# Kernel tuning notes

Hardware: AMD Instinct MI355X
Metric: run time of the kernel (lower is better)

## Reference

```python
import jax, jax.numpy as jnp
import numpy as np

B, N, G = 16, 6000, 256
T = 200                     # TRAIN_ROIS_PER_IMAGE
RATIO = 0.33                # POSITIVE_ROI_RATIO
POS_NUM = int(T * RATIO)    # 66 positive slots
NEG_SLOTS = T - POS_NUM     # 134 negative slots
BBOX_STD = jnp.asarray([0.1, 0.1, 0.2, 0.2], jnp.float32)
EPS = 1e-8


def _rand_boxes(key, b, n):
    # valid [y1,x1,y2,x2] boxes in [0,1]
    k1, k2 = jax.random.split(key)
    tl = jax.random.uniform(k1, (b, n, 2)) * 0.7
    wh = jax.random.uniform(k2, (b, n, 2)) * 0.25 + 0.02
    return jnp.concatenate([tl, tl + wh], axis=-1).astype(jnp.float32)


def setup_inputs() -> dict:
    key = jax.random.key(0)
    k1, k2, k3, k4, k5 = jax.random.split(key, 5)
    rois = _rand_boxes(k1, B, N)
    rois = rois.at[:, N - 1000:].set(0.0)          # zero padding tail (remove_zero_padding)
    gt_boxes = _rand_boxes(k2, B, G)
    gt_ids = jax.random.randint(k3, (B, G), 1, 81, dtype=jnp.int32)
    gt_ids = gt_ids.at[:, G - 32:G - 16].set(-1)   # crowd boxes (ids < 0)
    gt_ids = gt_ids.at[:, G - 16:].set(0)          # padded gt
    gt_boxes = gt_boxes.at[:, G - 16:].set(0.0)
    pos_score = jax.random.uniform(k4, (B, N), dtype=jnp.float32)
    neg_score = jax.random.uniform(k5, (B, N), dtype=jnp.float32)
    return {"rois": rois, "gt_ids": gt_ids, "gt_boxes": gt_boxes,
            "pos_score": pos_score, "neg_score": neg_score}


def _pairwise_iou(a, b):
    # a:[N,4], b:[G,4] -> [N,G]
    y1 = jnp.maximum(a[:, None, 0], b[None, :, 0])
    x1 = jnp.maximum(a[:, None, 1], b[None, :, 1])
    y2 = jnp.minimum(a[:, None, 2], b[None, :, 2])
    x2 = jnp.minimum(a[:, None, 3], b[None, :, 3])
    inter = jnp.clip(y2 - y1, 0.0) * jnp.clip(x2 - x1, 0.0)
    area_a = (a[:, 2] - a[:, 0]) * (a[:, 3] - a[:, 1])
    area_b = (b[:, 2] - b[:, 0]) * (b[:, 3] - b[:, 1])
    union = area_a[:, None] + area_b[None, :] - inter
    return inter / jnp.maximum(union, EPS)


def _bbox_offset(boxes, gt):
    h = jnp.maximum(boxes[:, 2] - boxes[:, 0], EPS)
    w = jnp.maximum(boxes[:, 3] - boxes[:, 1], EPS)
    cy = boxes[:, 0] + 0.5 * h
    cx = boxes[:, 1] + 0.5 * w
    gh = jnp.maximum(gt[:, 2] - gt[:, 0], EPS)
    gw = jnp.maximum(gt[:, 3] - gt[:, 1], EPS)
    gcy = gt[:, 0] + 0.5 * gh
    gcx = gt[:, 1] + 0.5 * gw
    off = jnp.stack([(gcy - cy) / h, (gcx - cx) / w,
                     jnp.log(gh / h), jnp.log(gw / w)], axis=1)
    return off / BBOX_STD


def _per_image(rois, gt_ids, gt_boxes, pos_score, neg_score):
    roi_valid = jnp.any(rois != 0.0, axis=1)        # [N]
    gt_valid = jnp.any(gt_boxes != 0.0, axis=1)     # [G]
    crowd = gt_valid & (gt_ids < 0)
    non_crowd = gt_valid & (gt_ids > 0)

    iou = _pairwise_iou(rois, gt_boxes)             # [N,G]
    iou_nc = jnp.where(non_crowd[None, :], iou, -1.0)
    iou_nc_max = jnp.max(iou_nc, axis=1)
    iou_cr_max = jnp.max(jnp.where(crowd[None, :], iou, 0.0), axis=1)

    pos_mask = roi_valid & (iou_nc_max >= 0.5)
    neg_mask = roi_valid & (iou_nc_max < 0.5) & (iou_cr_max < 0.001)

    # random sampling == sort by iid uniform scores (masked out -> -inf)
    pos_idx = jnp.argsort(-jnp.where(pos_mask, pos_score, -jnp.inf))[:POS_NUM]
    pos_count = jnp.minimum(jnp.sum(pos_mask), POS_NUM).astype(jnp.int32)
    pos_slot_valid = jnp.arange(POS_NUM) < pos_count

    neg_target = (jnp.float32(1.0 / RATIO) * pos_count.astype(jnp.float32)).astype(jnp.int32) - pos_count
    neg_idx = jnp.argsort(-jnp.where(neg_mask, neg_score, -jnp.inf))[:NEG_SLOTS]
    neg_count = jnp.minimum(jnp.sum(neg_mask).astype(jnp.int32),
                            jnp.minimum(neg_target, NEG_SLOTS))
    neg_slot_valid = jnp.arange(NEG_SLOTS) < neg_count

    pos_rois_raw = rois[pos_idx]                                   # [P,4]
    pos_rois = jnp.where(pos_slot_valid[:, None], pos_rois_raw, 0.0)
    neg_rois = jnp.where(neg_slot_valid[:, None], rois[neg_idx], 0.0)

    assign = jnp.argmax(iou_nc[pos_idx], axis=1)                   # gt assignment
    roi_gt_boxes = gt_boxes[assign]
    roi_gt_ids = jnp.where(pos_slot_valid, gt_ids[assign], 0)

    off = _bbox_offset(pos_rois_raw, roi_gt_boxes)
    off = jnp.where(pos_slot_valid[:, None], off, 0.0)

    out_rois = jnp.concatenate([pos_rois, neg_rois], axis=0)       # [T,4]
    out_ids = jnp.pad(roi_gt_ids, (0, NEG_SLOTS))                  # [T]
    out_off = jnp.pad(off, ((0, NEG_SLOTS), (0, 0)))               # [T,4]
    return out_rois, out_ids, out_off


def reference(rois, gt_ids, gt_boxes, pos_score, neg_score):
    return jax.vmap(_per_image)(rois, gt_ids, gt_boxes, pos_score, neg_score)
```

## Files before the change

kernel.cpp:

```cpp
#include <hip/hip_runtime.h>

#define BIMG 16
#define NROI 6000
#define NGT  256
#define TPOS 66
#define TNEG 134
#define TTOT 200
#define EPSF 1e-8f
#define INVALID_SCORE 0xFFFFFFFFu

#define CPB 2
#define UNITSB 94
#define P1_BLOCKS (UNITSB * BIMG)
#define NWAIT (2 * BIMG)
#define NT 256
#define VSLOTS 6
#define CAND_CAP 384

#define MAGIC1 0x9E3779B9u
#define MAGIC2 0x85EBCA77u

typedef unsigned long long u64;
typedef unsigned int u32;
typedef unsigned short u16;

struct P1Shared {
    float4 ncbox[NGT];
    float4 crbox[NGT];
    u16    gmap[NGT];
    int    wnc[4], wcr[4];
};

struct SelShared {
    u32 hist[2048];
    u32 wtot[4];
    u32 wsuf[4];
    int pick;
    u32 higher;
    u32 pickpop;
    u32 count;
    u64 comp[CAND_CAP];
    int cnt;
    int sel[TNEG];
};

__device__ __forceinline__ void phase1_block(
    int unit,
    const float* __restrict__ rois, const int* __restrict__ gt_ids,
    const float* __restrict__ gt_boxes, const float* __restrict__ pos_score,
    const float* __restrict__ neg_score, u32* __restrict__ pos_s,
    u32* __restrict__ neg_s, u32* __restrict__ assign, u32* __restrict__ flags,
    P1Shared& S)
{
#pragma clang fp contract(off)
    const int b = unit / UNITSB;
    const int u = unit - b * UNITSB;

    const int r_local = threadIdx.x >> 3;
    const int sub = threadIdx.x & 7;

    const float4* rois4 = (const float4*)rois + (size_t)b * NROI;
    float4 rbk[CPB];
    float  psk[CPB], nsk[CPB];
    int    nk[CPB];
#pragma unroll
    for (int k = 0; k < CPB; ++k) {
        int n = (u * CPB + k) * 32 + r_local;
        nk[k] = n;
        int ne = min(n, NROI - 1);
        rbk[k] = rois4[ne];
        psk[k] = 0.f; nsk[k] = 0.f;
        if (sub == 0) {
            psk[k] = pos_score[b * NROI + ne];
            nsk[k] = neg_score[b * NROI + ne];
        }
    }

    {
        const int g = threadIdx.x;
        const int lane = g & 63, w = g >> 6;
        float4 gb = ((const float4*)gt_boxes)[b * NGT + g];
        bool valid = (gb.x != 0.f) || (gb.y != 0.f) || (gb.z != 0.f) || (gb.w != 0.f);
        int id = gt_ids[b * NGT + g];
        bool isnc = valid && (id > 0);
        bool iscr = valid && (id < 0);
        u64 mnc = __ballot(isnc);
        u64 mcr = __ballot(iscr);
        if (lane == 0) { S.wnc[w] = (int)__popcll(mnc); S.wcr[w] = (int)__popcll(mcr); }
        __syncthreads();
        int offnc = 0, offcr = 0;
        for (int j = 0; j < w; ++j) { offnc += S.wnc[j]; offcr += S.wcr[j]; }
        u64 below = (lane == 0) ? 0ull : (~0ull >> (64 - lane));
        if (isnc) {
            int slot = offnc + (int)__popcll(mnc & below);
            S.ncbox[slot] = gb;
            S.gmap[slot] = (u16)g;
        }
        if (iscr) {
            int slot = offcr + (int)__popcll(mcr & below);
            S.crbox[slot] = gb;
        }
    }
    __syncthreads();
    const int nccnt = S.wnc[0] + S.wnc[1] + S.wnc[2] + S.wnc[3];
    const int crcnt = S.wcr[0] + S.wcr[1] + S.wcr[2] + S.wcr[3];

#pragma unroll
    for (int k = 0; k < CPB; ++k) {
        const float4 rb = rbk[k];
        const int n = nk[k];
        const bool rvalid = (rb.x != 0.f) || (rb.y != 0.f) || (rb.z != 0.f) || (rb.w != 0.f);
        const float area_a = (rb.z - rb.x) * (rb.w - rb.y);

        float best = -1.0f;
        float bsl  = 0.0f;
        float crmax = 0.0f;

        if (__ballot(rvalid) != 0ull) {
            auto step = [&](int i) {
                float4 p0 = S.ncbox[i];
                float y1 = fmaxf(rb.x, p0.x);
                float x1 = fmaxf(rb.y, p0.y);
                float y2 = fminf(rb.z, p0.z);
                float x2 = fminf(rb.w, p0.w);
                float ih = fmaxf(y2 - y1, 0.0f);
                float iw = fmaxf(x2 - x1, 0.0f);
                float inter = ih * iw;
                float ab = (p0.z - p0.x) * (p0.w - p0.y);
                float uni = fmaxf(area_a + ab - inter, EPSF);
                float iou = inter / uni;
                if (iou > best) { best = iou; bsl = (float)i; }
            };
            int i = sub;
            for (; i + 8 < nccnt; i += 16) { step(i); step(i + 8); }
            if (i < nccnt) step(i);

            for (int j = sub; j < crcnt; j += 8) {
                float4 p0 = S.crbox[j];
                float y1 = fmaxf(rb.x, p0.x);
                float x1 = fmaxf(rb.y, p0.y);
                float y2 = fminf(rb.z, p0.z);
                float x2 = fminf(rb.w, p0.w);
                float ih = fmaxf(y2 - y1, 0.0f);
                float iw = fmaxf(x2 - x1, 0.0f);
                float inter = ih * iw;
                float ab = (p0.z - p0.x) * (p0.w - p0.y);
                float uni = fmaxf(area_a + ab - inter, EPSF);
                crmax = fmaxf(crmax, inter / uni);
            }

            for (int m = 1; m <= 4; m <<= 1) {
                float ov = __shfl_xor(best, m);
                float os = __shfl_xor(bsl, m);
                float oc = __shfl_xor(crmax, m);
                if ((ov > best) || ((ov == best) && (os < bsl))) { best = ov; bsl = os; }
                crmax = fmaxf(crmax, oc);
            }
        }

        if (sub == 0 && n < NROI) {
            u32 ps = INVALID_SCORE, ns = INVALID_SCORE;
            if (rvalid) {
                if (best >= 0.5f)
                    ps = __float_as_uint(psk[k]);
                if ((best < 0.5f) && (crmax < 0.001f))
                    ns = __float_as_uint(nsk[k]);
            }
            int gsel = (nccnt > 0) ? (int)S.gmap[(int)bsl] : 0;
            __hip_atomic_store(&pos_s[b * NROI + n], ps,
                               __ATOMIC_RELAXED, __HIP_MEMORY_SCOPE_AGENT);
            __hip_atomic_store(&neg_s[b * NROI + n], ns,
                               __ATOMIC_RELAXED, __HIP_MEMORY_SCOPE_AGENT);
            __hip_atomic_store(&assign[b * NROI + n], (u32)gsel,
                               __ATOMIC_RELAXED, __HIP_MEMORY_SCOPE_AGENT);
        }
    }

    __syncthreads();
    if (threadIdx.x == 0) {
        __hip_atomic_store(&flags[2 * unit],     MAGIC1,
                           __ATOMIC_RELAXED, __HIP_MEMORY_SCOPE_AGENT);
        __hip_atomic_store(&flags[2 * unit + 1], MAGIC2,
                           __ATOMIC_RELAXED, __HIP_MEMORY_SCOPE_AGENT);
    }
}

__device__ __forceinline__ int count_valid(const u32* __restrict__ src,
                                           int tid, int lane, SelShared* S)
{
    const uint4* src4 = (const uint4*)src;
    int myvalid = 0;
#pragma unroll
    for (int s = 0; s < VSLOTS; ++s) {
        int vi = s * NT + tid;
        uint4 v = src4[vi];
        int base = vi * 4;
        myvalid += (base + 0 < NROI && v.x != INVALID_SCORE);
        myvalid += (base + 1 < NROI && v.y != INVALID_SCORE);
        myvalid += (base + 2 < NROI && v.z != INVALID_SCORE);
        myvalid += (base + 3 < NROI && v.w != INVALID_SCORE);
    }
    for (int off = 1; off < 64; off <<= 1) myvalid += __shfl_xor(myvalid, off);
    if (tid == 0) S->count = 0;
    __syncthreads();
    if (lane == 0) atomicAdd(&S->count, (u32)myvalid);
    __syncthreads();
    int tot = (int)S->count;
    __syncthreads();
    return tot;
}

__device__ __forceinline__ int radix_select(const u32* __restrict__ src, int K,
                                            int tid, int lane, int w, SelShared* S)
{
    const uint4* src4 = (const uint4*)src;
    int myvalid = 0;
#pragma unroll
    for (int s = 0; s < VSLOTS; ++s) {
        int vi = s * NT + tid;
        uint4 v = src4[vi];
        int base = vi * 4;
        myvalid += (base + 0 < NROI && v.x != INVALID_SCORE);
        myvalid += (base + 1 < NROI && v.y != INVALID_SCORE);
        myvalid += (base + 2 < NROI && v.z != INVALID_SCORE);
        myvalid += (base + 3 < NROI && v.w != INVALID_SCORE);
    }
    for (int off = 1; off < 64; off <<= 1) myvalid += __shfl_xor(myvalid, off);
    if (tid == 0) S->count = 0;
    __syncthreads();
    if (lane == 0) atomicAdd(&S->count, (u32)myvalid);
    __syncthreads();
    const int total = (int)S->count;
    const int K0 = min(K, total);
    if (K0 <= 0) return total;

    int Krem = K0;
    u64 prefix = 0ull, mask = 0ull;
    int cand = total;

    for (int p = 3; p >= 0; --p) {
        if (cand <= CAND_CAP) break;
        const int shift = p * 11;
        for (int i = tid; i < 2048; i += NT) S->hist[i] = 0;
        __syncthreads();
#pragma unroll
        for (int s = 0; s < VSLOTS; ++s) {
            int vi = s * NT + tid;
            uint4 v = src4[vi];
            int base = vi * 4;
            u32 vv[4] = {v.x, v.y, v.z, v.w};
#pragma unroll
            for (int j = 0; j < 4; ++j) {
                int idx = base + j;
                if (idx < NROI && vv[j] != INVALID_SCORE) {
                    u64 kk = ((u64)vv[j] << 13) | (u64)(8191 - idx);
                    if ((kk & mask) == prefix)
                        atomicAdd(&S->hist[(u32)(kk >> shift) & 2047u], 1u);
                }
            }
        }
        __syncthreads();
        u32 local = 0;
#pragma unroll
        for (int j = 0; j < 8; ++j) local += S->hist[8 * tid + j];
        u32 suf = local;
        for (int off = 1; off < 64; off <<= 1) {
            u32 v = __shfl_down(suf, off);
            if (lane + off < 64) suf += v;
        }
        if (lane == 0) S->wtot[w] = suf;
        __syncthreads();
        if (tid < 4) {
            u32 t = 0;
            for (int j = tid + 1; j < 4; ++j) t += S->wtot[j];
            S->wsuf[tid] = t;
        }
        __syncthreads();
        u32 Sincl = suf + S->wsuf[w];
        for (int k2 = 0; k2 < 8; ++k2) {
            u32 h = S->hist[8 * tid + k2];
            u32 Snext = Sincl - h;
            if (Sincl >= (u32)Krem && Snext < (u32)Krem) {
                S->pick = 8 * tid + k2;
                S->higher = Snext;
                S->pickpop = h;
            }
            Sincl = Snext;
        }
        __syncthreads();
        prefix |= ((u64)(u32)S->pick) << shift;
        mask   |= (2047ull << shift);
        Krem   -= (int)S->higher;
        cand    = (K0 - Krem) + (int)S->pickpop;
        __syncthreads();
    }

    if (tid == 0) S->cnt = 0;
    __syncthreads();
#pragma unroll
    for (int s = 0; s < VSLOTS; ++s) {
        int vi = s * NT + tid;
        uint4 v = src4[vi];
        int base = vi * 4;
        u32 vv[4] = {v.x, v.y, v.z, v.w};
#pragma unroll
        for (int j = 0; j < 4; ++j) {
            int idx = base + j;
            if (idx < NROI && vv[j] != INVALID_SCORE) {
                u64 kk = ((u64)vv[j] << 13) | (u64)(8191 - idx);
                if ((kk & mask) >= prefix) {
                    int pos = atomicAdd(&S->cnt, 1);
                    S->comp[pos] = kk;
                }
            }
        }
    }
    __syncthreads();
    const int Cnt = S->cnt;
    for (int c0 = tid; c0 < Cnt; c0 += NT) {
        u64 kk = S->comp[c0];
        int rank = 0;
        for (int j = 0; j < Cnt; ++j) rank += (S->comp[j] > kk);
        if (rank < K0) S->sel[rank] = 8191 - (int)(kk & 8191ull);
    }
    __syncthreads();
    return total;
}

__device__ __forceinline__ void phase2_block(
    int wbid,
    const float* __restrict__ rois, const int* __restrict__ gt_ids,
    const float* __restrict__ gt_boxes, const u32* __restrict__ pos_s,
    const u32* __restrict__ neg_s, const u32* __restrict__ assign,
    const u32* __restrict__ flags, float* __restrict__ out, SelShared& S)
{
#pragma clang fp contract(off)
    __shared__ int s_ndone;
    const int b = wbid >> 1;
    const int side = wbid & 1;
    const int tid = threadIdx.x;
    const int lane = tid & 63;
    const int w = tid >> 6;

    const u32* fb = flags + 2 * (b * UNITSB);
    int mydone = (tid < UNITSB) ? 0 : 1;
    for (;;) {
        if (tid == 0) s_ndone = 0;
        __syncthreads();
        if (!mydone) {
            u32 a = __hip_atomic_load(&fb[2 * tid],
                                      __ATOMIC_RELAXED, __HIP_MEMORY_SCOPE_AGENT);
            u32 c = __hip_atomic_load(&fb[2 * tid + 1],
                                      __ATOMIC_RELAXED, __HIP_MEMORY_SCOPE_AGENT);
            mydone = (a == MAGIC1 && c == MAGIC2);
        }
        int d = mydone;
        for (int off = 1; off < 64; off <<= 1) d += __shfl_xor(d, off);
        if (lane == 0) atomicAdd(&s_ndone, d);
        __syncthreads();
        if (s_ndone == NT) break;
        __builtin_amdgcn_s_sleep(8);
    }
    if (tid == 0)
        (void)__hip_atomic_load(&fb[0], __ATOMIC_ACQUIRE, __HIP_MEMORY_SCOPE_AGENT);
    __syncthreads();

    float* out_rois = out;
    float* out_ids  = out + BIMG * TTOT * 4;
    float* out_off  = out + BIMG * TTOT * 4 + BIMG * TTOT;

    if (side == 0) {
        const int pos_total = radix_select(pos_s + (size_t)b * NROI, TPOS,
                                           tid, lane, w, &S);
        const int pos_count = min(pos_total, TPOS);

        if (tid < TPOS) {
            const int base = b * TTOT + tid;
            float4 ro  = make_float4(0.f, 0.f, 0.f, 0.f);
            float  idv = 0.f;
            float4 off = make_float4(0.f, 0.f, 0.f, 0.f);
            if (tid < pos_count) {
                int n = S.sel[tid];
                float4 rb = ((const float4*)rois)[b * NROI + n];
                ro = rb;
                int g = (int)assign[b * NROI + n];
                float4 gb = ((const float4*)gt_boxes)[b * NGT + g];
                idv = (float)gt_ids[b * NGT + g];

                float h  = fmaxf(rb.z - rb.x, EPSF);
                float wd = fmaxf(rb.w - rb.y, EPSF);
                float cy = rb.x + 0.5f * h;
                float cx = rb.y + 0.5f * wd;
                float gh = fmaxf(gb.z - gb.x, EPSF);
                float gw = fmaxf(gb.w - gb.y, EPSF);
                float gcy = gb.x + 0.5f * gh;
                float gcx = gb.y + 0.5f * gw;
                off.x = ((gcy - cy) / h)  / 0.1f;
                off.y = ((gcx - cx) / wd) / 0.1f;
                off.z = logf(gh / h)  / 0.2f;
                off.w = logf(gw / wd) / 0.2f;
            }
            ((float4*)out_rois)[base] = ro;
            out_ids[base] = idv;
            ((float4*)out_off)[base] = off;
        }
    } else {
        const int pos_total = count_valid(pos_s + (size_t)b * NROI, tid, lane, &S);
        const int pos_count = min(pos_total, TPOS);
        const float ratio_inv = (float)(1.0 / 0.33);
        const int neg_target = (int)(ratio_inv * (float)pos_count) - pos_count;

        const int neg_total = radix_select(neg_s + (size_t)b * NROI, TNEG,
                                           tid, lane, w, &S);
        const int neg_count = max(0, min(neg_total, min(neg_target, TNEG)));

        if (tid < TNEG) {
            const int base = b * TTOT + TPOS + tid;
            float4 ro = make_float4(0.f, 0.f, 0.f, 0.f);
            if (tid < neg_count) {
                int n = S.sel[tid];
                ro = ((const float4*)rois)[b * NROI + n];
            }
            ((float4*)out_rois)[base] = ro;
            out_ids[base] = 0.f;
            ((float4*)out_off)[base] = make_float4(0.f, 0.f, 0.f, 0.f);
        }
    }
}

__global__ __launch_bounds__(NT, 4)
void fused_kernel(const float* __restrict__ rois,
                  const int* __restrict__ gt_ids,
                  const float* __restrict__ gt_boxes,
                  const float* __restrict__ pos_score,
                  const float* __restrict__ neg_score,
                  u32* __restrict__ pos_s,
                  u32* __restrict__ neg_s,
                  u32* __restrict__ assign,
                  u32* __restrict__ flags,
                  float* __restrict__ out)
{
    constexpr size_t SB = sizeof(P1Shared) > sizeof(SelShared)
                        ? sizeof(P1Shared) : sizeof(SelShared);
    __shared__ __align__(16) char smem[SB];

    if (blockIdx.x >= NWAIT) {
        phase1_block((int)blockIdx.x - NWAIT, rois, gt_ids, gt_boxes, pos_score,
                     neg_score, pos_s, neg_s, assign, flags,
                     *reinterpret_cast<P1Shared*>(smem));
    } else {
        phase2_block((int)blockIdx.x, rois, gt_ids, gt_boxes,
                     pos_s, neg_s, assign, flags, out,
                     *reinterpret_cast<SelShared*>(smem));
    }
}

extern "C" void kernel_launch(void* const* d_in, const int* in_sizes, int n_in,
                              void* d_out, int out_size, void* d_ws, size_t ws_size,
                              hipStream_t stream) {
    const float* rois      = (const float*)d_in[0];
    const int*   gt_ids    = (const int*)d_in[1];
    const float* gt_boxes  = (const float*)d_in[2];
    const float* pos_score = (const float*)d_in[3];
    const float* neg_score = (const float*)d_in[4];
    float* out = (float*)d_out;

    char* ws = (char*)d_ws;
    u32* pos_s  = (u32*)(ws + 0);
    u32* neg_s  = (u32*)(ws + 384000);
    u32* assign = (u32*)(ws + 768000);
    u32* flags  = (u32*)(ws + 1152000);

    fused_kernel<<<NWAIT + P1_BLOCKS, NT, 0, stream>>>(
        rois, gt_ids, gt_boxes, pos_score, neg_score,
        pos_s, neg_s, assign, flags, out);
}
```

Before: 96.76 us.

## Map one ROI per thread in phase 1 and precompute GT areas

Phase 1 now gives each thread a whole ROI and loops over all GT boxes itself, replacing the old scheme of 8 threads per ROI followed by a shuffle reduction. The number of phase-1 blocks per image falls from 94 to 24. GT box areas are computed once and stored in shared memory instead of being recomputed for every pair. This removes the shuffle reductions and the redundant area math, but it cuts block count and parallelism, so each thread runs a loop about 8x longer and the grid may not fill the GPU.

```diff
diff --git a/kernel.cpp b/kernel.cpp
--- a/kernel.cpp
+++ b/kernel.cpp
@@ -9,8 +9,8 @@
 #define EPSF 1e-8f
 #define INVALID_SCORE 0xFFFFFFFFu
 
-#define CPB 2
-#define UNITSB 94
+#define RPB 256
+#define UNITSB 24
 #define P1_BLOCKS (UNITSB * BIMG)
 #define NWAIT (2 * BIMG)
 #define NT 256
@@ -26,7 +26,9 @@
 
 struct P1Shared {
     float4 ncbox[NGT];
+    float  ncarea[NGT];
     float4 crbox[NGT];
+    float  crarea[NGT];
     u16    gmap[NGT];
     int    wnc[4], wcr[4];
 };
@@ -55,33 +57,21 @@
 #pragma clang fp contract(off)
     const int b = unit / UNITSB;
     const int u = unit - b * UNITSB;
-
-    const int r_local = threadIdx.x >> 3;
-    const int sub = threadIdx.x & 7;
-
-    const float4* rois4 = (const float4*)rois + (size_t)b * NROI;
-    float4 rbk[CPB];
-    float  psk[CPB], nsk[CPB];
-    int    nk[CPB];
-#pragma unroll
-    for (int k = 0; k < CPB; ++k) {
-        int n = (u * CPB + k) * 32 + r_local;
-        nk[k] = n;
-        int ne = min(n, NROI - 1);
-        rbk[k] = rois4[ne];
-        psk[k] = 0.f; nsk[k] = 0.f;
-        if (sub == 0) {
-            psk[k] = pos_score[b * NROI + ne];
-            nsk[k] = neg_score[b * NROI + ne];
-        }
-    }
+    const int tid = threadIdx.x;
+
+    const int n = u * RPB + tid;
+    const int ne = min(n, NROI - 1);
+    const float4 rb = ((const float4*)rois)[b * NROI + ne];
+    const float ps_in = pos_score[b * NROI + ne];
+    const float ns_in = neg_score[b * NROI + ne];
 
     {
-        const int g = threadIdx.x;
+        const int g = tid;
         const int lane = g & 63, w = g >> 6;
         float4 gb = ((const float4*)gt_boxes)[b * NGT + g];
         bool valid = (gb.x != 0.f) || (gb.y != 0.f) || (gb.z != 0.f) || (gb.w != 0.f);
         int id = gt_ids[b * NGT + g];
+        float area = (gb.z - gb.x) * (gb.w - gb.y);
         bool isnc = valid && (id > 0);
         bool iscr = valid && (id < 0);
         u64 mnc = __ballot(isnc);
@@ -94,90 +84,76 @@
         if (isnc) {
             int slot = offnc + (int)__popcll(mnc & below);
             S.ncbox[slot] = gb;
+            S.ncarea[slot] = area;
             S.gmap[slot] = (u16)g;
         }
         if (iscr) {
             int slot = offcr + (int)__popcll(mcr & below);
             S.crbox[slot] = gb;
+            S.crarea[slot] = area;
         }
     }
     __syncthreads();
     const int nccnt = S.wnc[0] + S.wnc[1] + S.wnc[2] + S.wnc[3];
     const int crcnt = S.wcr[0] + S.wcr[1] + S.wcr[2] + S.wcr[3];
 
-#pragma unroll
-    for (int k = 0; k < CPB; ++k) {
-        const float4 rb = rbk[k];
-        const int n = nk[k];
-        const bool rvalid = (rb.x != 0.f) || (rb.y != 0.f) || (rb.z != 0.f) || (rb.w != 0.f);
+    const bool rvalid = (rb.x != 0.f) || (rb.y != 0.f) || (rb.z != 0.f) || (rb.w != 0.f);
+    float best = -1.0f;
+    int   bsl  = 0;
+    float crmax = 0.0f;
+
+    if (rvalid) {
         const float area_a = (rb.z - rb.x) * (rb.w - rb.y);
-
-        float best = -1.0f;
-        float bsl  = 0.0f;
-        float crmax = 0.0f;
-
-        if (__ballot(rvalid) != 0ull) {
-            auto step = [&](int i) {
-                float4 p0 = S.ncbox[i];
-                float y1 = fmaxf(rb.x, p0.x);
-                float x1 = fmaxf(rb.y, p0.y);
-                float y2 = fminf(rb.z, p0.z);
-                float x2 = fminf(rb.w, p0.w);
-                float ih = fmaxf(y2 - y1, 0.0f);
-                float iw = fmaxf(x2 - x1, 0.0f);
-                float inter = ih * iw;
-                float ab = (p0.z - p0.x) * (p0.w - p0.y);
-                float uni = fmaxf(area_a + ab - inter, EPSF);
-                float iou = inter / uni;
-                if (iou > best) { best = iou; bsl = (float)i; }
-            };
-            int i = sub;
-            for (; i + 8 < nccnt; i += 16) { step(i); step(i + 8); }
-            if (i < nccnt) step(i);
-
-            for (int j = sub; j < crcnt; j += 8) {
-                float4 p0 = S.crbox[j];
-                float y1 = fmaxf(rb.x, p0.x);
-                float x1 = fmaxf(rb.y, p0.y);
-                float y2 = fminf(rb.z, p0.z);
-                float x2 = fminf(rb.w, p0.w);
-                float ih = fmaxf(y2 - y1, 0.0f);
-                float iw = fmaxf(x2 - x1, 0.0f);
-                float inter = ih * iw;
-                float ab = (p0.z - p0.x) * (p0.w - p0.y);
-                float uni = fmaxf(area_a + ab - inter, EPSF);
-                crmax = fmaxf(crmax, inter / uni);
-            }
-
-            for (int m = 1; m <= 4; m <<= 1) {
-                float ov = __shfl_xor(best, m);
-                float os = __shfl_xor(bsl, m);
-                float oc = __shfl_xor(crmax, m);
-                if ((ov > best) || ((ov == best) && (os < bsl))) { best = ov; bsl = os; }
-                crmax = fmaxf(crmax, oc);
-            }
-        }
-
-        if (sub == 0 && n < NROI) {
-            u32 ps = INVALID_SCORE, ns = INVALID_SCORE;
-            if (rvalid) {
-                if (best >= 0.5f)
-                    ps = __float_as_uint(psk[k]);
-                if ((best < 0.5f) && (crmax < 0.001f))
-                    ns = __float_as_uint(nsk[k]);
-            }
-            int gsel = (nccnt > 0) ? (int)S.gmap[(int)bsl] : 0;
-            __hip_atomic_store(&pos_s[b * NROI + n], ps,
-                               __ATOMIC_RELAXED, __HIP_MEMORY_SCOPE_AGENT);
-            __hip_atomic_store(&neg_s[b * NROI + n], ns,
-                               __ATOMIC_RELAXED, __HIP_MEMORY_SCOPE_AGENT);
-            __hip_atomic_store(&assign[b * NROI + n], (u32)gsel,
-                               __ATOMIC_RELAXED, __HIP_MEMORY_SCOPE_AGENT);
-        }
-    }
-
-    __syncthreads();
-    if (threadIdx.x == 0) {
+#pragma unroll 4
+        for (int i = 0; i < nccnt; ++i) {
+            float4 p0 = S.ncbox[i];
+            float  ab = S.ncarea[i];
+            float y1 = fmaxf(rb.x, p0.x);
+            float x1 = fmaxf(rb.y, p0.y);
+            float y2 = fminf(rb.z, p0.z);
+            float x2 = fminf(rb.w, p0.w);
+            float ih = fmaxf(y2 - y1, 0.0f);
+            float iw = fmaxf(x2 - x1, 0.0f);
+            float inter = ih * iw;
+            float uni = fmaxf(area_a + ab - inter, EPSF);
+            float iou = inter / uni;
+            if (iou > best) { best = iou; bsl = i; }
+        }
+#pragma unroll 4
+        for (int i = 0; i < crcnt; ++i) {
+            float4 p0 = S.crbox[i];
+            float  ab = S.crarea[i];
+            float y1 = fmaxf(rb.x, p0.x);
+            float x1 = fmaxf(rb.y, p0.y);
+            float y2 = fminf(rb.z, p0.z);
+            float x2 = fminf(rb.w, p0.w);
+            float ih = fmaxf(y2 - y1, 0.0f);
+            float iw = fmaxf(x2 - x1, 0.0f);
+            float inter = ih * iw;
+            float uni = fmaxf(area_a + ab - inter, EPSF);
+            crmax = fmaxf(crmax, inter / uni);
+        }
+    }
+
+    if (n < NROI) {
+        u32 ps = INVALID_SCORE, ns = INVALID_SCORE;
+        if (rvalid) {
+            if (best >= 0.5f)
+                ps = __float_as_uint(ps_in);
+            if ((best < 0.5f) && (crmax < 0.001f))
+                ns = __float_as_uint(ns_in);
+        }
+        int gsel = (nccnt > 0) ? (int)S.gmap[bsl] : 0;
+        __hip_atomic_store(&pos_s[b * NROI + n], ps,
+                           __ATOMIC_RELAXED, __HIP_MEMORY_SCOPE_AGENT);
+        __hip_atomic_store(&neg_s[b * NROI + n], ns,
+                           __ATOMIC_RELAXED, __HIP_MEMORY_SCOPE_AGENT);
+        __hip_atomic_store(&assign[b * NROI + n], (u32)gsel,
+                           __ATOMIC_RELAXED, __HIP_MEMORY_SCOPE_AGENT);
+    }
+
+    __syncthreads();
+    if (tid == 0) {
         __hip_atomic_store(&flags[2 * unit],     MAGIC1,
                            __ATOMIC_RELAXED, __HIP_MEMORY_SCOPE_AGENT);
         __hip_atomic_store(&flags[2 * unit + 1], MAGIC2,
@@ -380,10 +356,10 @@
             float  idv = 0.f;
             float4 off = make_float4(0.f, 0.f, 0.f, 0.f);
             if (tid < pos_count) {
-                int n = S.sel[tid];
-                float4 rb = ((const float4*)rois)[b * NROI + n];
+                int nn = S.sel[tid];
+                float4 rb = ((const float4*)rois)[b * NROI + nn];
                 ro = rb;
-                int g = (int)assign[b * NROI + n];
+                int g = (int)assign[b * NROI + nn];
                 float4 gb = ((const float4*)gt_boxes)[b * NGT + g];
                 idv = (float)gt_ids[b * NGT + g];
 
@@ -418,8 +394,8 @@
             const int base = b * TTOT + TPOS + tid;
             float4 ro = make_float4(0.f, 0.f, 0.f, 0.f);
             if (tid < neg_count) {
-                int n = S.sel[tid];
-                ro = ((const float4*)rois)[b * NROI + n];
+                int nn = S.sel[tid];
+                ro = ((const float4*)rois)[b * NROI + nn];
             }
             ((float4*)out_rois)[base] = ro;
             out_ids[base] = 0.f;
```

Result: slower. 101.6 us (+5.0%).
